# Kernel optimization log

Hardware: AMD Instinct MI355X
Metric: run time of the kernel (lower is better)

The kernel has to match this reference:

```python
import jax, jax.numpy as jnp
import numpy as np

N, D, K, P = 4096, 256, 16, 3
MAXDEG = K + 1          # self loop guarantees deg >= 1, randint caps deg <= K+1
TAU, LAM, BETA, MARGIN = 0.8, 0.5, 1.0, 0.1
EPS_PD = 1e-6           # F.pairwise_distance eps (added to the difference)


def _make_adj(k):
    nbr = jax.random.randint(k, (N, K), 0, N)
    m = jnp.zeros((N, N), jnp.float32)
    m = m.at[jnp.arange(N)[:, None], nbr].set(1.0)
    m = m.at[jnp.arange(N), jnp.arange(N)].set(1.0)
    return m / m.sum(1, keepdims=True)  # row-normalized metapath adjacency


def setup_inputs():
    key = jax.random.key(0)
    ks = jax.random.split(key, 12)
    g = 1.414 * (2.0 / (D + D)) ** 0.5  # xavier_normal gain=1.414
    return {
        "h": jax.random.normal(ks[0], (N, D), jnp.float32),
        "mps": jnp.stack([_make_adj(ks[1 + i]) for i in range(P)]),
        "W_gcn": jax.random.normal(ks[4], (P, D, D), jnp.float32) * g,
        "b_gcn": jnp.zeros((P, D), jnp.float32),
        "prelu_a": jnp.full((P,), 0.25, jnp.float32),
        "att_fc_W": jax.random.normal(ks[5], (D, D), jnp.float32) * g,
        "att_fc_b": jnp.zeros((D,), jnp.float32),
        "att_vec": jax.random.normal(ks[6], (D,), jnp.float32) * g,
        "proj_W1": jax.random.normal(ks[7], (D, D), jnp.float32) * g,
        "proj_b1": jnp.zeros((D,), jnp.float32),
        "proj_W2": jax.random.normal(ks[8], (D, D), jnp.float32) * g,
        "proj_b2": jnp.zeros((D,), jnp.float32),
    }


def _gcn(h, adj, W, b, a):
    out = adj @ (h @ W.T) + b          # spmm(adj, fc(h)) + bias
    return jnp.where(out > 0, out, a * out)  # PReLU


def _node_loss(emb, adj):
    # vectorized form of the per-node nonzero/pairwise_distance loop
    mask = adj > 0                      # [N, N]
    deg = mask.sum(1)                   # [N], >= 1 via self loops
    # stable argsort: neighbors first (ascending index), matching torch.nonzero order
    pos_idx = jnp.argsort(~mask, axis=1)[:, :MAXDEG]
    neg_idx = jnp.argsort(mask, axis=1)[:, :MAXDEG]   # first deg non-neighbors
    anc = emb[:, None, :]               # anchor expanded over pairs
    dp = jnp.sum((anc - emb[pos_idx] + EPS_PD) ** 2, -1)  # [N, MAXDEG]
    dn = jnp.sum((anc - emb[neg_idx] + EPS_PD) ** 2, -1)
    valid = jnp.arange(MAXDEG)[None, :] < deg[:, None]
    per = jnp.maximum(dp - dn + MARGIN, 0.0) * valid
    return jnp.sum(per.sum(1) / deg.astype(emb.dtype))  # per-node mean, summed


def _proj(z, W1, b1, W2, b2):
    return jax.nn.elu(z @ W1.T + b1) @ W2.T + b2


def _contrast(z1, z2, pos, W1, b1, W2, b2):
    p1 = _proj(z1, W1, b1, W2, b2)
    p2 = _proj(z2, W1, b1, W2, b2)
    n1 = jnp.linalg.norm(p1, axis=-1, keepdims=True)
    n2 = jnp.linalg.norm(p2, axis=-1, keepdims=True)
    sim = jnp.exp((p1 @ p2.T) / (n1 * n2.T) / TAU)     # [N, N]
    m12 = sim / (sim.sum(1, keepdims=True) + 1e-8)
    m21 = sim.T / (sim.T.sum(1, keepdims=True) + 1e-8)
    l12 = -jnp.log((m12 * pos).sum(-1)).mean()
    l21 = -jnp.log((m21 * pos).sum(-1)).mean()
    return LAM * l12 + (1.0 - LAM) * l21


def reference(h, mps, W_gcn, b_gcn, prelu_a, att_fc_W, att_fc_b, att_vec,
              proj_W1, proj_b1, proj_W2, proj_b2):
    embeds = [_gcn(h, mps[i], W_gcn[i], b_gcn[i], prelu_a[i]) for i in range(P)]
    node_loss = sum(_node_loss(embeds[i], mps[i]) for i in range(P))
    # faithful to original control flow: i==0 inner loop overwrites self.loss,
    # so only the (0, P-1) pair survives from i==0
    closs = _contrast(embeds[0], embeds[P - 1], mps[0], proj_W1, proj_b1, proj_W2, proj_b2)
    for i in range(1, P - 1):
        for j in range(i + 1, P):
            closs = closs + _contrast(embeds[i], embeds[j], mps[i], proj_W1, proj_b1, proj_W2, proj_b2)
    # semantic attention over metapaths
    sp = jnp.stack([jnp.tanh(e @ att_fc_W.T + att_fc_b).mean(0) for e in embeds])  # [P, D]
    beta = jax.nn.softmax(sp @ att_vec)                                            # [P]
    z_mp = jnp.einsum('p,pnd->nd', beta, jnp.stack(embeds))
    return z_mp, node_loss + BETA * closs
```

## Files before the change

### kernel.cpp

```cpp
#include <hip/hip_runtime.h>
#include <hip/hip_bf16.h>

constexpr int N = 4096;
constexpr int D = 256;
constexpr int P = 3;
constexpr int MAXDEG = 17;
constexpr float TAU = 0.8f;
constexpr float MARGIN = 0.1f;
constexpr float EPS_PD = 1e-6f;

constexpr int LDP = 40;
constexpr int LDK = 72;

constexpr int OFF_H    = 0;
constexpr int OFF_WG   = 1048576;
constexpr int OFF_ATTW = 1245184;
constexpr int OFF_W1   = 1310720;
constexpr int OFF_W2   = 1376256;
constexpr int OFF_BG   = 1441792;
constexpr int OFF_ATTB = 1442560;
constexpr int OFF_AV   = 1442816;
constexpr int OFF_PA   = 1443072;
constexpr int OFF_B1   = 1443328;
constexpr int OFF_B2   = 1443584;
constexpr int CONV_TOTAL = 1443840;

typedef __attribute__((ext_vector_type(8))) short bfrag8;
typedef __attribute__((ext_vector_type(4))) float facc4;

__device__ inline facc4 mfma16(bfrag8 a, bfrag8 b, facc4 c) {
    return __builtin_amdgcn_mfma_f32_16x16x32_bf16(a, b, c, 0, 0, 0);
}
__device__ inline float b2f(__hip_bfloat16 v) { return __bfloat162float(v); }
__device__ inline float bfbits2f(unsigned short u) {
    return __uint_as_float(((unsigned int)u) << 16);
}
__device__ inline unsigned short f2bfbits(float v) {
    __hip_bfloat16 t = __float2bfloat16(v);
    return *(unsigned short*)&t;
}
__device__ inline int get_bf(const int* __restrict__ counter) { return counter[0] > 100; }

__device__ inline float load_in(const void* p, size_t i, int bf) {
    return bf ? __bfloat162float(((const __hip_bfloat16*)p)[i])
              : ((const float*)p)[i];
}

__global__ void detect_dtype(const unsigned int* __restrict__ w, int nwords,
                             int* __restrict__ counter) {
    int stride = gridDim.x * blockDim.x;
    int c = 0;
    for (int i = blockIdx.x * blockDim.x + threadIdx.x; i < nwords; i += stride) {
        unsigned int x = w[i];
        if ((x & 0xFFFF0000u) == 0u && x != 0u) c++;
    }
    for (int s = 32; s > 0; s >>= 1) c += __shfl_down(c, s);
    if ((threadIdx.x & 63) == 0 && c > 0) atomicAdd(counter, c);
}

__global__ void convert_all(const void* h, const void* wg, const void* attw,
                            const void* w1, const void* w2, const void* bg,
                            const void* attb, const void* av, const void* pa,
                            const void* b1, const void* b2,
                            const int* __restrict__ counter,
                            __hip_bfloat16* __restrict__ dst) {
    int bf = get_bf(counter);
    const void* srcs[11] = {h, wg, attw, w1, w2, bg, attb, av, pa, b1, b2};
    const int offs[11] = {OFF_H, OFF_WG, OFF_ATTW, OFF_W1, OFF_W2, OFF_BG,
                          OFF_ATTB, OFF_AV, OFF_PA, OFF_B1, OFF_B2};
    const int lens[11] = {1048576, 196608, 65536, 65536, 65536, 768, 256, 256, 3, 256, 256};
    int stride = gridDim.x * blockDim.x;
    int t0 = blockIdx.x * blockDim.x + threadIdx.x;
    #pragma unroll
    for (int s = 0; s < 11; s++) {
        for (int i = t0; i < lens[s]; i += stride)
            dst[offs[s] + i] = __float2bfloat16(load_in(srcs[s], i, bf));
    }
}

__global__ void extract_sparse(const void* __restrict__ mps, const int* __restrict__ counter,
                               int* __restrict__ nbr_idx, float* __restrict__ nbr_val,
                               int* __restrict__ neg_idx, int* __restrict__ deg) {
    int bf = get_bf(counter);
    int row = blockIdx.x;
    int t = threadIdx.x;
    __shared__ int cnt;
    __shared__ int sidx[32];
    __shared__ float sval[32];
    if (t == 0) cnt = 0;
    __syncthreads();
    int e0 = t * 16;
    if (bf) {
        const uint4* base = (const uint4*)((const __hip_bfloat16*)mps + (size_t)row * N + e0);
        #pragma unroll
        for (int v = 0; v < 2; v++) {
            uint4 w = base[v];
            unsigned int ws[4] = {w.x, w.y, w.z, w.w};
            #pragma unroll
            for (int j = 0; j < 4; j++) {
                unsigned short lo = (unsigned short)(ws[j] & 0xFFFFu);
                unsigned short hi = (unsigned short)(ws[j] >> 16);
                if (lo) { int k = atomicAdd(&cnt, 1); if (k < 32) { sidx[k] = e0 + v * 8 + j * 2;     sval[k] = bfbits2f(lo); } }
                if (hi) { int k = atomicAdd(&cnt, 1); if (k < 32) { sidx[k] = e0 + v * 8 + j * 2 + 1; sval[k] = bfbits2f(hi); } }
            }
        }
    } else {
        const float4* base = (const float4*)((const float*)mps + (size_t)row * N + e0);
        #pragma unroll
        for (int v = 0; v < 4; v++) {
            float4 w = base[v];
            float ws[4] = {w.x, w.y, w.z, w.w};
            #pragma unroll
            for (int j = 0; j < 4; j++)
                if (ws[j] > 0.f) { int k = atomicAdd(&cnt, 1); if (k < 32) { sidx[k] = e0 + v * 4 + j; sval[k] = ws[j]; } }
        }
    }
    __syncthreads();
    if (t == 0) {
        int dg = cnt; if (dg > MAXDEG) dg = MAXDEG;
        for (int i = 1; i < dg; i++) {
            int ki = sidx[i]; float kv = sval[i]; int j = i - 1;
            while (j >= 0 && sidx[j] > ki) { sidx[j+1] = sidx[j]; sval[j+1] = sval[j]; j--; }
            sidx[j+1] = ki; sval[j+1] = kv;
        }
        deg[row] = dg;
        int* oi = nbr_idx + (size_t)row * MAXDEG;
        float* ov = nbr_val + (size_t)row * MAXDEG;
        int* ng = neg_idx + (size_t)row * MAXDEG;
        for (int i = 0; i < MAXDEG; i++) { oi[i] = (i < dg) ? sidx[i] : 0; ov[i] = (i < dg) ? sval[i] : 0.f; }
        int c = 0, j = 0, found = 0;
        while (found < MAXDEG) {
            if (j < dg && sidx[j] == c) { j++; c++; continue; }
            ng[found++] = c++;
        }
    }
}

template <int ACT>
__global__ void gemm_mfma(const __hip_bfloat16* __restrict__ Abase, size_t strideA,
                          const __hip_bfloat16* __restrict__ Bbase, size_t strideB,
                          const __hip_bfloat16* __restrict__ bias, size_t strideBias,
                          __hip_bfloat16* __restrict__ Cbase, size_t strideC) {
    int z = blockIdx.z;
    const __hip_bfloat16* A = Abase + (size_t)z * strideA;
    const __hip_bfloat16* B = Bbase + (size_t)z * strideB;
    __shared__ __align__(16) __hip_bfloat16 As[64 * LDP];
    __shared__ __align__(16) __hip_bfloat16 Bs[64 * LDP];
    int bm = blockIdx.x * 64, bn = blockIdx.y * 64;
    int tid = threadIdx.x, wave = tid >> 6, lane = tid & 63;
    int quad = lane >> 4, l15 = lane & 15;
    int wr = (wave & 1) * 32, wc = (wave >> 1) * 32;
    facc4 acc[2][2] = {};
    int sr = tid >> 2, kq = (tid & 3) * 8;
    for (int k0 = 0; k0 < D; k0 += 32) {
        *(bfrag8*)&As[sr * LDP + kq] = *(const bfrag8*)&A[(size_t)(bm + sr) * D + k0 + kq];
        *(bfrag8*)&Bs[sr * LDP + kq] = *(const bfrag8*)&B[(size_t)(bn + sr) * D + k0 + kq];
        __syncthreads();
        bfrag8 af[2], bfr[2];
        #pragma unroll
        for (int mi = 0; mi < 2; mi++)
            af[mi] = *(const bfrag8*)&As[(wr + mi * 16 + l15) * LDP + quad * 8];
        #pragma unroll
        for (int ni = 0; ni < 2; ni++)
            bfr[ni] = *(const bfrag8*)&Bs[(wc + ni * 16 + l15) * LDP + quad * 8];
        #pragma unroll
        for (int mi = 0; mi < 2; mi++)
            #pragma unroll
            for (int ni = 0; ni < 2; ni++)
                acc[mi][ni] = mfma16(af[mi], bfr[ni], acc[mi][ni]);
        __syncthreads();
    }
    #pragma unroll
    for (int mi = 0; mi < 2; mi++) {
        #pragma unroll
        for (int ni = 0; ni < 2; ni++) {
            int col = bn + wc + ni * 16 + l15;
            #pragma unroll
            for (int r = 0; r < 4; r++) {
                int row = bm + wr + mi * 16 + quad * 4 + r;
                float v = acc[mi][ni][r];
                if (bias) v += b2f(bias[col]);
                if (ACT == 1) v = v > 0.f ? v : expm1f(v);
                Cbase[(size_t)z * strideC + (size_t)row * D + col] = __float2bfloat16(v);
            }
        }
    }
}

__global__ void gemm_dual(const __hip_bfloat16* __restrict__ embBase,
                          const __hip_bfloat16* __restrict__ conv,
                          __hip_bfloat16* __restrict__ xbuf,
                          float* __restrict__ spacc) {
    int z = blockIdx.z;
    const __hip_bfloat16* A = embBase + (size_t)z * N * D;
    const __hip_bfloat16* Ba = conv + OFF_ATTW;
    const __hip_bfloat16* Bw = conv + OFF_W1;
    __shared__ __align__(16) __hip_bfloat16 As[64 * LDP];
    __shared__ __align__(16) __hip_bfloat16 Bsa[64 * LDP];
    __shared__ __align__(16) __hip_bfloat16 Bsw[64 * LDP];
    int bm = blockIdx.x * 64, bn = blockIdx.y * 64;
    int tid = threadIdx.x, wave = tid >> 6, lane = tid & 63;
    int quad = lane >> 4, l15 = lane & 15;
    int wr = (wave & 1) * 32, wc = (wave >> 1) * 32;
    facc4 accA[2][2] = {};
    facc4 accW[2][2] = {};
    int sr = tid >> 2, kq = (tid & 3) * 8;
    for (int k0 = 0; k0 < D; k0 += 32) {
        *(bfrag8*)&As[sr * LDP + kq]  = *(const bfrag8*)&A[(size_t)(bm + sr) * D + k0 + kq];
        *(bfrag8*)&Bsa[sr * LDP + kq] = *(const bfrag8*)&Ba[(size_t)(bn + sr) * D + k0 + kq];
        *(bfrag8*)&Bsw[sr * LDP + kq] = *(const bfrag8*)&Bw[(size_t)(bn + sr) * D + k0 + kq];
        __syncthreads();
        bfrag8 af[2], ba[2], bw[2];
        #pragma unroll
        for (int mi = 0; mi < 2; mi++)
            af[mi] = *(const bfrag8*)&As[(wr + mi * 16 + l15) * LDP + quad * 8];
        #pragma unroll
        for (int ni = 0; ni < 2; ni++) {
            ba[ni] = *(const bfrag8*)&Bsa[(wc + ni * 16 + l15) * LDP + quad * 8];
            bw[ni] = *(const bfrag8*)&Bsw[(wc + ni * 16 + l15) * LDP + quad * 8];
        }
        #pragma unroll
        for (int mi = 0; mi < 2; mi++)
            #pragma unroll
            for (int ni = 0; ni < 2; ni++) {
                accA[mi][ni] = mfma16(af[mi], ba[ni], accA[mi][ni]);
                accW[mi][ni] = mfma16(af[mi], bw[ni], accW[mi][ni]);
            }
        __syncthreads();
    }
    float cs[2] = {0.f, 0.f};
    #pragma unroll
    for (int mi = 0; mi < 2; mi++) {
        #pragma unroll
        for (int ni = 0; ni < 2; ni++) {
            int col = bn + wc + ni * 16 + l15;
            float battb = b2f(conv[OFF_ATTB + col]);
            float bb1   = b2f(conv[OFF_B1 + col]);
            #pragma unroll
            for (int r = 0; r < 4; r++) {
                int row = bm + wr + mi * 16 + quad * 4 + r;
                cs[ni] += tanhf(accA[mi][ni][r] + battb);
                float v = accW[mi][ni][r] + bb1;
                v = v > 0.f ? v : expm1f(v);
                xbuf[(size_t)z * N * D + (size_t)row * D + col] = __float2bfloat16(v);
            }
        }
    }
    #pragma unroll
    for (int ni = 0; ni < 2; ni++) {
        float v = cs[ni];
        v += __shfl_xor(v, 16); v += __shfl_xor(v, 32);
        if (quad == 0) {
            int col = bn + wc + ni * 16 + l15;
            atomicAdd(&spacc[(size_t)z * D + col], v);
        }
    }
}

__global__ void gemm_w2_norm(const __hip_bfloat16* __restrict__ xbase,
                             const __hip_bfloat16* __restrict__ conv,
                             __hip_bfloat16* __restrict__ qbase) {
    int z = blockIdx.z;
    const __hip_bfloat16* A = xbase + (size_t)z * N * D;
    const __hip_bfloat16* B = conv + OFF_W2;
    __shared__ __align__(16) __hip_bfloat16 As[16 * LDP];
    __shared__ __align__(16) __hip_bfloat16 Bs[256 * LDP];
    __shared__ float sred[4][16];
    int bm = blockIdx.x * 16;
    int tid = threadIdx.x, wave = tid >> 6, lane = tid & 63;
    int quad = lane >> 4, l15 = lane & 15;
    int wc = wave * 64;
    facc4 acc[4] = {};
    for (int k0 = 0; k0 < D; k0 += 32) {
        if (tid < 64) {
            int r = tid >> 2, kq = (tid & 3) * 8;
            *(bfrag8*)&As[r * LDP + kq] = *(const bfrag8*)&A[(size_t)(bm + r) * D + k0 + kq];
        }
        #pragma unroll
        for (int i = 0; i < 4; i++) {
            int f = tid + 256 * i;
            int r = f >> 2, kq = (f & 3) * 8;
            *(bfrag8*)&Bs[r * LDP + kq] = *(const bfrag8*)&B[(size_t)r * D + k0 + kq];
        }
        __syncthreads();
        bfrag8 af = *(const bfrag8*)&As[l15 * LDP + quad * 8];
        #pragma unroll
        for (int ni = 0; ni < 4; ni++) {
            bfrag8 bf = *(const bfrag8*)&Bs[(wc + ni * 16 + l15) * LDP + quad * 8];
            acc[ni] = mfma16(af, bf, acc[ni]);
        }
        __syncthreads();
    }
    float vv[4][4];
    #pragma unroll
    for (int ni = 0; ni < 4; ni++) {
        float bb = b2f(conv[OFF_B2 + wc + ni * 16 + l15]);
        #pragma unroll
        for (int r = 0; r < 4; r++) vv[ni][r] = acc[ni][r] + bb;
    }
    #pragma unroll
    for (int r = 0; r < 4; r++) {
        float ss = vv[0][r] * vv[0][r] + vv[1][r] * vv[1][r] +
                   vv[2][r] * vv[2][r] + vv[3][r] * vv[3][r];
        ss += __shfl_xor(ss, 1); ss += __shfl_xor(ss, 2);
        ss += __shfl_xor(ss, 4); ss += __shfl_xor(ss, 8);
        if (l15 == 0) sred[wave][quad * 4 + r] = ss;
    }
    __syncthreads();
    #pragma unroll
    for (int r = 0; r < 4; r++) {
        int rl = quad * 4 + r;
        float ssum = sred[0][rl] + sred[1][rl] + sred[2][rl] + sred[3][rl];
        float inv = rsqrtf(ssum + 1e-30f);
        int row = bm + rl;
        #pragma unroll
        for (int ni = 0; ni < 4; ni++)
            qbase[(size_t)z * N * D + (size_t)row * D + wc + ni * 16 + l15] =
                __float2bfloat16(vv[ni][r] * inv);
    }
}

__global__ void spmm_prelu(const __hip_bfloat16* __restrict__ Xbase,
                           const int* __restrict__ nbr_idx, const float* __restrict__ nbr_val,
                           const int* __restrict__ deg, const __hip_bfloat16* __restrict__ conv,
                           __hip_bfloat16* __restrict__ embBase) {
    int z = blockIdx.z;
    int wave = threadIdx.x >> 6, lane = threadIdx.x & 63;
    int n = blockIdx.x * 4 + wave;
    const __hip_bfloat16* X = Xbase + (size_t)z * N * D;
    const int* idx = nbr_idx + ((size_t)z * N + n) * MAXDEG;
    const float* val = nbr_val + ((size_t)z * N + n) * MAXDEG;
    int dg = deg[z * N + n];
    float acc[4] = {0.f, 0.f, 0.f, 0.f};
    for (int k = 0; k < dg; k++) {
        int j = idx[k];
        float vk = val[k];
        ushort4 x = *(const ushort4*)&X[(size_t)j * D + lane * 4];
        acc[0] += vk * bfbits2f(x.x); acc[1] += vk * bfbits2f(x.y);
        acc[2] += vk * bfbits2f(x.z); acc[3] += vk * bfbits2f(x.w);
    }
    ushort4 bb = *(const ushort4*)&conv[OFF_BG + z * D + lane * 4];
    float b[4] = {bfbits2f(bb.x), bfbits2f(bb.y), bfbits2f(bb.z), bfbits2f(bb.w)};
    float a = b2f(conv[OFF_PA + z]);
    ushort4 o;
    float v0 = acc[0] + b[0]; o.x = f2bfbits(v0 > 0.f ? v0 : a * v0);
    float v1 = acc[1] + b[1]; o.y = f2bfbits(v1 > 0.f ? v1 : a * v1);
    float v2 = acc[2] + b[2]; o.z = f2bfbits(v2 > 0.f ? v2 : a * v2);
    float v3 = acc[3] + b[3]; o.w = f2bfbits(v3 > 0.f ? v3 : a * v3);
    *(ushort4*)&embBase[(size_t)z * N * D + (size_t)n * D + lane * 4] = o;
}

__global__ void sim_mfma(const __hip_bfloat16* __restrict__ q,
                         float* __restrict__ rowsum, float* __restrict__ colsum) {
    int pair = blockIdx.z;
    const __hip_bfloat16* Qa = q + (size_t)pair * N * D;
    const __hip_bfloat16* Qb = q + (size_t)2 * N * D;
    __shared__ __align__(16) __hip_bfloat16 As[128 * LDK];
    __shared__ __align__(16) __hip_bfloat16 Bs[128 * LDK];
    int bm = blockIdx.x * 128, bn = blockIdx.y * 128;
    int tid = threadIdx.x, wave = tid >> 6, lane = tid & 63;
    int quad = lane >> 4, l15 = lane & 15;
    int wr = (wave & 1) * 64, wc = (wave >> 1) * 64;
    facc4 acc[4][4] = {};
    int sr0 = tid >> 3, kq = (tid & 7) * 8;
    for (int k0 = 0; k0 < D; k0 += 64) {
        #pragma unroll
        for (int i = 0; i < 4; i++) {
            int r = sr0 + 32 * i;
            *(bfrag8*)&As[r * LDK + kq] = *(const bfrag8*)&Qa[(size_t)(bm + r) * D + k0 + kq];
            *(bfrag8*)&Bs[r * LDK + kq] = *(const bfrag8*)&Qb[(size_t)(bn + r) * D + k0 + kq];
        }
        __syncthreads();
        #pragma unroll
        for (int kk = 0; kk < 64; kk += 32) {
            bfrag8 af[4], bfr[4];
            #pragma unroll
            for (int mi = 0; mi < 4; mi++)
                af[mi] = *(const bfrag8*)&As[(wr + mi * 16 + l15) * LDK + kk + quad * 8];
            #pragma unroll
            for (int ni = 0; ni < 4; ni++)
                bfr[ni] = *(const bfrag8*)&Bs[(wc + ni * 16 + l15) * LDK + kk + quad * 8];
            #pragma unroll
            for (int mi = 0; mi < 4; mi++)
                #pragma unroll
                for (int ni = 0; ni < 4; ni++)
                    acc[mi][ni] = mfma16(af[mi], bfr[ni], acc[mi][ni]);
        }
        __syncthreads();
    }
    constexpr float invtau = 1.0f / TAU;
    float rs[4][4];
    float cs[4] = {0.f, 0.f, 0.f, 0.f};
    #pragma unroll
    for (int mi = 0; mi < 4; mi++)
        #pragma unroll
        for (int r = 0; r < 4; r++) rs[mi][r] = 0.f;
    #pragma unroll
    for (int mi = 0; mi < 4; mi++)
        #pragma unroll
        for (int ni = 0; ni < 4; ni++)
            #pragma unroll
            for (int r = 0; r < 4; r++) {
                float e = __expf(acc[mi][ni][r] * invtau);
                rs[mi][r] += e;
                cs[ni] += e;
            }
    #pragma unroll
    for (int mi = 0; mi < 4; mi++)
        #pragma unroll
        for (int r = 0; r < 4; r++) {
            float v = rs[mi][r];
            v += __shfl_xor(v, 1); v += __shfl_xor(v, 2);
            v += __shfl_xor(v, 4); v += __shfl_xor(v, 8);
            rs[mi][r] = v;
        }
    if (l15 == 0) {
        #pragma unroll
        for (int mi = 0; mi < 4; mi++)
            #pragma unroll
            for (int r = 0; r < 4; r++)
                atomicAdd(&rowsum[(size_t)pair * N + bm + wr + mi * 16 + quad * 4 + r], rs[mi][r]);
    }
    #pragma unroll
    for (int ni = 0; ni < 4; ni++) {
        float v = cs[ni];
        v += __shfl_xor(v, 16); v += __shfl_xor(v, 32);
        if (quad == 0)
            atomicAdd(&colsum[(size_t)pair * N + bn + wc + ni * 16 + l15], v);
    }
}

__global__ void posdot(const __hip_bfloat16* __restrict__ q,
                       const int* __restrict__ nbr_idx, const float* __restrict__ nbr_val,
                       const int* __restrict__ deg,
                       float* __restrict__ pdrow, float* __restrict__ pdcol) {
    int pair = blockIdx.z;
    int wave = threadIdx.x >> 6, lane = threadIdx.x & 63;
    int n = blockIdx.x * 4 + wave;
    const __hip_bfloat16* Qa = q + (size_t)pair * N * D;
    const __hip_bfloat16* Qb = q + (size_t)2 * N * D;
    int dg = deg[pair * N + n];
    const int* idx = nbr_idx + ((size_t)pair * N + n) * MAXDEG;
    const float* val = nbr_val + ((size_t)pair * N + n) * MAXDEG;
    const float invtau = 1.0f / TAU;
    ushort4 ar = *(const ushort4*)&Qa[(size_t)n * D + lane * 4];
    ushort4 br = *(const ushort4*)&Qb[(size_t)n * D + lane * 4];
    float a[4] = {bfbits2f(ar.x), bfbits2f(ar.y), bfbits2f(ar.z), bfbits2f(ar.w)};
    float b[4] = {bfbits2f(br.x), bfbits2f(br.y), bfbits2f(br.z), bfbits2f(br.w)};
    float sr = 0.f, sc = 0.f;
    for (int k = 0; k < dg; k++) {
        int j = idx[k];
        ushort4 pj = *(const ushort4*)&Qb[(size_t)j * D + lane * 4];
        ushort4 aj = *(const ushort4*)&Qa[(size_t)j * D + lane * 4];
        float dr = a[0] * bfbits2f(pj.x) + a[1] * bfbits2f(pj.y) +
                   a[2] * bfbits2f(pj.z) + a[3] * bfbits2f(pj.w);
        float dc = b[0] * bfbits2f(aj.x) + b[1] * bfbits2f(aj.y) +
                   b[2] * bfbits2f(aj.z) + b[3] * bfbits2f(aj.w);
        #pragma unroll
        for (int s = 1; s <= 32; s <<= 1) { dr += __shfl_xor(dr, s); dc += __shfl_xor(dc, s); }
        sr += __expf(dr * invtau) * val[k];
        sc += __expf(dc * invtau) * val[k];
    }
    if (lane == 0) { pdrow[pair * N + n] = sr; pdcol[pair * N + n] = sc; }
}

__global__ void node_loss_k(const __hip_bfloat16* __restrict__ embBase,
                            const int* __restrict__ nbr_idx, const int* __restrict__ neg_idx,
                            const int* __restrict__ deg, float* __restrict__ nlpart) {
    int z = blockIdx.z;
    int wave = threadIdx.x >> 6, lane = threadIdx.x & 63;
    int n = blockIdx.x * 4 + wave;
    const __hip_bfloat16* emb = embBase + (size_t)z * N * D;
    int dg = deg[z * N + n];
    const int* ip = nbr_idx + ((size_t)z * N + n) * MAXDEG;
    const int* ig = neg_idx + ((size_t)z * N + n) * MAXDEG;
    ushort4 ar = *(const ushort4*)&emb[(size_t)n * D + lane * 4];
    float a[4] = {bfbits2f(ar.x), bfbits2f(ar.y), bfbits2f(ar.z), bfbits2f(ar.w)};
    float s = 0.f;
    for (int k = 0; k < dg; k++) {
        int jp = ip[k], jn = ig[k];
        ushort4 pr = *(const ushort4*)&emb[(size_t)jp * D + lane * 4];
        ushort4 nr = *(const ushort4*)&emb[(size_t)jn * D + lane * 4];
        float pv[4] = {bfbits2f(pr.x), bfbits2f(pr.y), bfbits2f(pr.z), bfbits2f(pr.w)};
        float nv[4] = {bfbits2f(nr.x), bfbits2f(nr.y), bfbits2f(nr.z), bfbits2f(nr.w)};
        float dp = 0.f, dn = 0.f;
        #pragma unroll
        for (int i = 0; i < 4; i++) {
            float x = a[i] - pv[i] + EPS_PD; dp += x * x;
            float y = a[i] - nv[i] + EPS_PD; dn += y * y;
        }
        #pragma unroll
        for (int st = 1; st <= 32; st <<= 1) { dp += __shfl_xor(dp, st); dn += __shfl_xor(dn, st); }
        float v = dp - dn + MARGIN;
        s += v > 0.f ? v : 0.f;
    }
    if (lane == 0) nlpart[z * N + n] = s / (float)dg;
}

__global__ void reduce_loss_beta(const float* __restrict__ nlpart,
                                 const float* __restrict__ rowsum, const float* __restrict__ colsum,
                                 const float* __restrict__ pdrow, const float* __restrict__ pdcol,
                                 const float* __restrict__ spacc,
                                 const __hip_bfloat16* __restrict__ conv,
                                 float* __restrict__ beta, float* __restrict__ loss) {
    int t = threadIdx.x;
    __shared__ float red[256];
    __shared__ float w[P];
    for (int p = 0; p < P; p++) {
        float v = (spacc[p * D + t] / (float)N) * b2f(conv[OFF_AV + t]);
        red[t] = v;
        __syncthreads();
        for (int s = 128; s > 0; s >>= 1) { if (t < s) red[t] += red[t + s]; __syncthreads(); }
        if (t == 0) w[p] = red[0];
        __syncthreads();
    }
    float s = 0.f;
    for (int i = t; i < P * N; i += 256) s += nlpart[i];
    for (int i = t; i < 2 * N; i += 256) {
        float l12 = -logf(pdrow[i] / (rowsum[i] + 1e-8f));
        float l21 = -logf(pdcol[i] / (colsum[i] + 1e-8f));
        s += (0.5f * l12 + 0.5f * l21) / (float)N;
    }
    red[t] = s;
    __syncthreads();
    for (int st = 128; st > 0; st >>= 1) { if (t < st) red[t] += red[t + st]; __syncthreads(); }
    if (t == 0) {
        loss[0] = red[0];
        float m = fmaxf(w[0], fmaxf(w[1], w[2]));
        float e0 = __expf(w[0] - m), e1 = __expf(w[1] - m), e2 = __expf(w[2] - m);
        float ssum = e0 + e1 + e2;
        beta[0] = e0 / ssum; beta[1] = e1 / ssum; beta[2] = e2 / ssum;
    }
}

__global__ void zmp_out(const __hip_bfloat16* __restrict__ embBase, const float* __restrict__ beta,
                        const float* __restrict__ loss, const int* __restrict__ counter,
                        void* __restrict__ out) {
    int bf = get_bf(counter);
    int i = blockIdx.x * 256 + threadIdx.x;
    float v = beta[0] * b2f(embBase[i]) + beta[1] * b2f(embBase[(size_t)N * D + i]) +
              beta[2] * b2f(embBase[(size_t)2 * N * D + i]);
    if (bf) {
        __hip_bfloat16* o = (__hip_bfloat16*)out;
        o[i] = __float2bfloat16(v);
        if (i == 0) o[(size_t)N * D] = __float2bfloat16(*loss);
    } else {
        float* o = (float*)out;
        o[i] = v;
        if (i == 0) o[(size_t)N * D] = *loss;
    }
}

extern "C" void kernel_launch(void* const* d_in, const int* in_sizes, int n_in,
                              void* d_out, int out_size, void* d_ws, size_t ws_size,
                              hipStream_t stream) {
    const void* h        = d_in[0];
    const void* mps      = d_in[1];
    const void* W_gcn    = d_in[2];
    const void* b_gcn    = d_in[3];
    const void* prelu_a  = d_in[4];
    const void* att_fc_W = d_in[5];
    const void* att_fc_b = d_in[6];
    const void* att_vec  = d_in[7];
    const void* proj_W1  = d_in[8];
    const void* proj_b1  = d_in[9];
    const void* proj_W2  = d_in[10];
    const void* proj_b2  = d_in[11];

    char* ws = (char*)d_ws;
    size_t off = 0;
    auto alloc = [&](size_t bytes) -> char* {
        char* p = ws + off;
        off = (off + bytes + 255) & ~(size_t)255;
        return p;
    };
    __hip_bfloat16* conv = (__hip_bfloat16*)alloc((size_t)CONV_TOTAL * 2);
    __hip_bfloat16* xbuf = (__hip_bfloat16*)alloc((size_t)P * N * D * 2);
    __hip_bfloat16* emb  = (__hip_bfloat16*)alloc((size_t)P * N * D * 2);
    __hip_bfloat16* q    = (__hip_bfloat16*)alloc((size_t)P * N * D * 2);
    int*   nbr_idx = (int*)alloc((size_t)P * N * MAXDEG * 4);
    float* nbr_val = (float*)alloc((size_t)P * N * MAXDEG * 4);
    int*   neg_idx = (int*)alloc((size_t)P * N * MAXDEG * 4);
    int*   deg     = (int*)alloc((size_t)P * N * 4);
    float* nlpart  = (float*)alloc((size_t)P * N * 4);
    float* pdrow   = (float*)alloc((size_t)2 * N * 4);
    float* pdcol   = (float*)alloc((size_t)2 * N * 4);
    char* zero_begin = ws + off;
    float* rowsum = (float*)alloc((size_t)2 * N * 4);
    float* colsum = (float*)alloc((size_t)2 * N * 4);
    float* spacc  = (float*)alloc((size_t)P * D * 4);
    float* beta   = (float*)alloc(16);
    float* loss   = (float*)alloc(16);
    int*   counter = (int*)alloc(16);
    size_t zero_bytes = (size_t)((ws + off) - zero_begin);
    hipMemsetAsync(zero_begin, 0, zero_bytes, stream);

    detect_dtype<<<1024, 256, 0, stream>>>((const unsigned int*)mps, 2 * 1024 * 1024, counter);

    convert_all<<<512, 256, 0, stream>>>(h, W_gcn, att_fc_W, proj_W1, proj_W2, b_gcn,
                                         att_fc_b, att_vec, prelu_a, proj_b1, proj_b2,
                                         counter, conv);

    extract_sparse<<<P * N, 256, 0, stream>>>(mps, counter, nbr_idx, nbr_val, neg_idx, deg);

    dim3 ggrid(N / 64, D / 64, P);
    size_t nd = (size_t)N * D;
    gemm_mfma<0><<<ggrid, 256, 0, stream>>>(
        conv + OFF_H, 0, conv + OFF_WG, (size_t)D * D, nullptr, 0, xbuf, nd);
    spmm_prelu<<<dim3(N / 4, 1, P), 256, 0, stream>>>(xbuf, nbr_idx, nbr_val, deg, conv, emb);
    gemm_dual<<<ggrid, 256, 0, stream>>>(emb, conv, xbuf, spacc);
    gemm_w2_norm<<<dim3(N / 16, 1, P), 256, 0, stream>>>(xbuf, conv, q);
    sim_mfma<<<dim3(N / 128, N / 128, 2), 256, 0, stream>>>(q, rowsum, colsum);
    posdot<<<dim3(N / 4, 1, 2), 256, 0, stream>>>(q, nbr_idx, nbr_val, deg, pdrow, pdcol);
    node_loss_k<<<dim3(N / 4, 1, P), 256, 0, stream>>>(emb, nbr_idx, neg_idx, deg, nlpart);
    reduce_loss_beta<<<1, 256, 0, stream>>>(nlpart, rowsum, colsum, pdrow, pdcol,
                                            spacc, conv, beta, loss);
    zmp_out<<<(N * D) / 256, 256, 0, stream>>>(emb, beta, loss, counter, d_out);
}
```

Before: 507.8 us.

## Use direct global-to-LDS loads with XOR swizzle in sim GEMM; merge edge kernels

The similarity GEMM now stages Q tiles with global_load_lds 16-byte transfers straight into LDS, using an XOR-swizzled unpadded layout instead of padded rows. This removes the register round-trip and uses the swizzle to avoid LDS bank conflicts. Separately, the posdot and node_loss kernels are merged into one launch over P+2 z-slices, which saves a kernel launch and lets the two gather workloads share the GPU. The swizzle indexing must match between store and read, and 16-byte global_load_lds support is hardware-specific.

```diff
diff --git a/kernel.cpp b/kernel.cpp
--- a/kernel.cpp
+++ b/kernel.cpp
@@ -10,7 +10,6 @@
 constexpr float EPS_PD = 1e-6f;
 
 constexpr int LDP = 40;
-constexpr int LDK = 72;
 
 constexpr int OFF_H    = 0;
 constexpr int OFF_WG   = 1048576;
@@ -44,6 +43,12 @@
 __device__ inline float load_in(const void* p, size_t i, int bf) {
     return bf ? __bfloat162float(((const __hip_bfloat16*)p)[i])
               : ((const float*)p)[i];
+}
+
+__device__ __forceinline__ void gl_lds16(const __hip_bfloat16* g, __hip_bfloat16* l) {
+    __builtin_amdgcn_global_load_lds(
+        (const __attribute__((address_space(1))) unsigned int*)g,
+        (__attribute__((address_space(3))) unsigned int*)l, 16, 0, 0);
 }
 
 __global__ void detect_dtype(const unsigned int* __restrict__ w, int nwords,
@@ -355,31 +360,40 @@
     int pair = blockIdx.z;
     const __hip_bfloat16* Qa = q + (size_t)pair * N * D;
     const __hip_bfloat16* Qb = q + (size_t)2 * N * D;
-    __shared__ __align__(16) __hip_bfloat16 As[128 * LDK];
-    __shared__ __align__(16) __hip_bfloat16 Bs[128 * LDK];
+    __shared__ __align__(16) __hip_bfloat16 As[128 * 64];
+    __shared__ __align__(16) __hip_bfloat16 Bs[128 * 64];
     int bm = blockIdx.x * 128, bn = blockIdx.y * 128;
     int tid = threadIdx.x, wave = tid >> 6, lane = tid & 63;
     int quad = lane >> 4, l15 = lane & 15;
     int wr = (wave & 1) * 64, wc = (wave >> 1) * 64;
     facc4 acc[4][4] = {};
-    int sr0 = tid >> 3, kq = (tid & 7) * 8;
+    int sr0 = tid >> 3;
+    int cc  = tid & 7;
     for (int k0 = 0; k0 < D; k0 += 64) {
         #pragma unroll
         for (int i = 0; i < 4; i++) {
             int r = sr0 + 32 * i;
-            *(bfrag8*)&As[r * LDK + kq] = *(const bfrag8*)&Qa[(size_t)(bm + r) * D + k0 + kq];
-            *(bfrag8*)&Bs[r * LDK + kq] = *(const bfrag8*)&Qb[(size_t)(bn + r) * D + k0 + kq];
+            int cg = (cc ^ (r & 7)) * 8;
+            gl_lds16(&Qa[(size_t)(bm + r) * D + k0 + cg], &As[r * 64 + cc * 8]);
+            gl_lds16(&Qb[(size_t)(bn + r) * D + k0 + cg], &Bs[r * 64 + cc * 8]);
         }
         __syncthreads();
         #pragma unroll
         for (int kk = 0; kk < 64; kk += 32) {
+            int kb = kk >> 3;
             bfrag8 af[4], bfr[4];
             #pragma unroll
-            for (int mi = 0; mi < 4; mi++)
-                af[mi] = *(const bfrag8*)&As[(wr + mi * 16 + l15) * LDK + kk + quad * 8];
-            #pragma unroll
-            for (int ni = 0; ni < 4; ni++)
-                bfr[ni] = *(const bfrag8*)&Bs[(wc + ni * 16 + l15) * LDK + kk + quad * 8];
+            for (int mi = 0; mi < 4; mi++) {
+                int R = wr + mi * 16 + l15;
+                int pc = ((kb + quad) ^ (l15 & 7)) * 8;
+                af[mi] = *(const bfrag8*)&As[R * 64 + pc];
+            }
+            #pragma unroll
+            for (int ni = 0; ni < 4; ni++) {
+                int R = wc + ni * 16 + l15;
+                int pc = ((kb + quad) ^ (l15 & 7)) * 8;
+                bfr[ni] = *(const bfrag8*)&Bs[R * 64 + pc];
+            }
             #pragma unroll
             for (int mi = 0; mi < 4; mi++)
                 #pragma unroll
@@ -430,71 +444,68 @@
     }
 }
 
-__global__ void posdot(const __hip_bfloat16* __restrict__ q,
-                       const int* __restrict__ nbr_idx, const float* __restrict__ nbr_val,
-                       const int* __restrict__ deg,
-                       float* __restrict__ pdrow, float* __restrict__ pdcol) {
-    int pair = blockIdx.z;
-    int wave = threadIdx.x >> 6, lane = threadIdx.x & 63;
-    int n = blockIdx.x * 4 + wave;
-    const __hip_bfloat16* Qa = q + (size_t)pair * N * D;
-    const __hip_bfloat16* Qb = q + (size_t)2 * N * D;
-    int dg = deg[pair * N + n];
-    const int* idx = nbr_idx + ((size_t)pair * N + n) * MAXDEG;
-    const float* val = nbr_val + ((size_t)pair * N + n) * MAXDEG;
-    const float invtau = 1.0f / TAU;
-    ushort4 ar = *(const ushort4*)&Qa[(size_t)n * D + lane * 4];
-    ushort4 br = *(const ushort4*)&Qb[(size_t)n * D + lane * 4];
-    float a[4] = {bfbits2f(ar.x), bfbits2f(ar.y), bfbits2f(ar.z), bfbits2f(ar.w)};
-    float b[4] = {bfbits2f(br.x), bfbits2f(br.y), bfbits2f(br.z), bfbits2f(br.w)};
-    float sr = 0.f, sc = 0.f;
-    for (int k = 0; k < dg; k++) {
-        int j = idx[k];
-        ushort4 pj = *(const ushort4*)&Qb[(size_t)j * D + lane * 4];
-        ushort4 aj = *(const ushort4*)&Qa[(size_t)j * D + lane * 4];
-        float dr = a[0] * bfbits2f(pj.x) + a[1] * bfbits2f(pj.y) +
-                   a[2] * bfbits2f(pj.z) + a[3] * bfbits2f(pj.w);
-        float dc = b[0] * bfbits2f(aj.x) + b[1] * bfbits2f(aj.y) +
-                   b[2] * bfbits2f(aj.z) + b[3] * bfbits2f(aj.w);
-        #pragma unroll
-        for (int s = 1; s <= 32; s <<= 1) { dr += __shfl_xor(dr, s); dc += __shfl_xor(dc, s); }
-        sr += __expf(dr * invtau) * val[k];
-        sc += __expf(dc * invtau) * val[k];
-    }
-    if (lane == 0) { pdrow[pair * N + n] = sr; pdcol[pair * N + n] = sc; }
-}
-
-__global__ void node_loss_k(const __hip_bfloat16* __restrict__ embBase,
-                            const int* __restrict__ nbr_idx, const int* __restrict__ neg_idx,
-                            const int* __restrict__ deg, float* __restrict__ nlpart) {
+__global__ void edge_losses(const __hip_bfloat16* __restrict__ embBase,
+                            const __hip_bfloat16* __restrict__ q,
+                            const int* __restrict__ nbr_idx, const float* __restrict__ nbr_val,
+                            const int* __restrict__ neg_idx, const int* __restrict__ deg,
+                            float* __restrict__ nlpart,
+                            float* __restrict__ pdrow, float* __restrict__ pdcol) {
     int z = blockIdx.z;
     int wave = threadIdx.x >> 6, lane = threadIdx.x & 63;
     int n = blockIdx.x * 4 + wave;
-    const __hip_bfloat16* emb = embBase + (size_t)z * N * D;
-    int dg = deg[z * N + n];
-    const int* ip = nbr_idx + ((size_t)z * N + n) * MAXDEG;
-    const int* ig = neg_idx + ((size_t)z * N + n) * MAXDEG;
-    ushort4 ar = *(const ushort4*)&emb[(size_t)n * D + lane * 4];
-    float a[4] = {bfbits2f(ar.x), bfbits2f(ar.y), bfbits2f(ar.z), bfbits2f(ar.w)};
-    float s = 0.f;
-    for (int k = 0; k < dg; k++) {
-        int jp = ip[k], jn = ig[k];
-        ushort4 pr = *(const ushort4*)&emb[(size_t)jp * D + lane * 4];
-        ushort4 nr = *(const ushort4*)&emb[(size_t)jn * D + lane * 4];
-        float pv[4] = {bfbits2f(pr.x), bfbits2f(pr.y), bfbits2f(pr.z), bfbits2f(pr.w)};
-        float nv[4] = {bfbits2f(nr.x), bfbits2f(nr.y), bfbits2f(nr.z), bfbits2f(nr.w)};
-        float dp = 0.f, dn = 0.f;
-        #pragma unroll
-        for (int i = 0; i < 4; i++) {
-            float x = a[i] - pv[i] + EPS_PD; dp += x * x;
-            float y = a[i] - nv[i] + EPS_PD; dn += y * y;
-        }
-        #pragma unroll
-        for (int st = 1; st <= 32; st <<= 1) { dp += __shfl_xor(dp, st); dn += __shfl_xor(dn, st); }
-        float v = dp - dn + MARGIN;
-        s += v > 0.f ? v : 0.f;
-    }
-    if (lane == 0) nlpart[z * N + n] = s / (float)dg;
+    if (z < P) {
+        const __hip_bfloat16* emb = embBase + (size_t)z * N * D;
+        int dg = deg[z * N + n];
+        const int* ip = nbr_idx + ((size_t)z * N + n) * MAXDEG;
+        const int* ig = neg_idx + ((size_t)z * N + n) * MAXDEG;
+        ushort4 ar = *(const ushort4*)&emb[(size_t)n * D + lane * 4];
+        float a[4] = {bfbits2f(ar.x), bfbits2f(ar.y), bfbits2f(ar.z), bfbits2f(ar.w)};
+        float s = 0.f;
+        for (int k = 0; k < dg; k++) {
+            int jp = ip[k], jn = ig[k];
+            ushort4 pr = *(const ushort4*)&emb[(size_t)jp * D + lane * 4];
+            ushort4 nr = *(const ushort4*)&emb[(size_t)jn * D + lane * 4];
+            float dp = 0.f, dn = 0.f;
+            float x0 = a[0] - bfbits2f(pr.x) + EPS_PD, y0 = a[0] - bfbits2f(nr.x) + EPS_PD;
+            float x1 = a[1] - bfbits2f(pr.y) + EPS_PD, y1 = a[1] - bfbits2f(nr.y) + EPS_PD;
+            float x2 = a[2] - bfbits2f(pr.z) + EPS_PD, y2 = a[2] - bfbits2f(nr.z) + EPS_PD;
+            float x3 = a[3] - bfbits2f(pr.w) + EPS_PD, y3 = a[3] - bfbits2f(nr.w) + EPS_PD;
+            dp = x0 * x0 + x1 * x1 + x2 * x2 + x3 * x3;
+            dn = y0 * y0 + y1 * y1 + y2 * y2 + y3 * y3;
+            #pragma unroll
+            for (int st = 1; st <= 32; st <<= 1) { dp += __shfl_xor(dp, st); dn += __shfl_xor(dn, st); }
+            float v = dp - dn + MARGIN;
+            s += v > 0.f ? v : 0.f;
+        }
+        if (lane == 0) nlpart[z * N + n] = s / (float)dg;
+    } else {
+        int pair = z - P;
+        const __hip_bfloat16* Qa = q + (size_t)pair * N * D;
+        const __hip_bfloat16* Qb = q + (size_t)2 * N * D;
+        int dg = deg[pair * N + n];
+        const int* idx = nbr_idx + ((size_t)pair * N + n) * MAXDEG;
+        const float* val = nbr_val + ((size_t)pair * N + n) * MAXDEG;
+        const float invtau = 1.0f / TAU;
+        ushort4 ar = *(const ushort4*)&Qa[(size_t)n * D + lane * 4];
+        ushort4 br = *(const ushort4*)&Qb[(size_t)n * D + lane * 4];
+        float a[4] = {bfbits2f(ar.x), bfbits2f(ar.y), bfbits2f(ar.z), bfbits2f(ar.w)};
+        float b[4] = {bfbits2f(br.x), bfbits2f(br.y), bfbits2f(br.z), bfbits2f(br.w)};
+        float sr = 0.f, sc = 0.f;
+        for (int k = 0; k < dg; k++) {
+            int j = idx[k];
+            ushort4 pj = *(const ushort4*)&Qb[(size_t)j * D + lane * 4];
+            ushort4 aj = *(const ushort4*)&Qa[(size_t)j * D + lane * 4];
+            float dr = a[0] * bfbits2f(pj.x) + a[1] * bfbits2f(pj.y) +
+                       a[2] * bfbits2f(pj.z) + a[3] * bfbits2f(pj.w);
+            float dc = b[0] * bfbits2f(aj.x) + b[1] * bfbits2f(aj.y) +
+                       b[2] * bfbits2f(aj.z) + b[3] * bfbits2f(aj.w);
+            #pragma unroll
+            for (int s = 1; s <= 32; s <<= 1) { dr += __shfl_xor(dr, s); dc += __shfl_xor(dc, s); }
+            sr += __expf(dr * invtau) * val[k];
+            sc += __expf(dc * invtau) * val[k];
+        }
+        if (lane == 0) { pdrow[pair * N + n] = sr; pdcol[pair * N + n] = sc; }
+    }
 }
 
 __global__ void reduce_loss_beta(const float* __restrict__ nlpart,
@@ -611,8 +622,8 @@
     gemm_dual<<<ggrid, 256, 0, stream>>>(emb, conv, xbuf, spacc);
     gemm_w2_norm<<<dim3(N / 16, 1, P), 256, 0, stream>>>(xbuf, conv, q);
     sim_mfma<<<dim3(N / 128, N / 128, 2), 256, 0, stream>>>(q, rowsum, colsum);
-    posdot<<<dim3(N / 4, 1, 2), 256, 0, stream>>>(q, nbr_idx, nbr_val, deg, pdrow, pdcol);
-    node_loss_k<<<dim3(N / 4, 1, P), 256, 0, stream>>>(emb, nbr_idx, neg_idx, deg, nlpart);
+    edge_losses<<<dim3(N / 4, 1, P + 2), 256, 0, stream>>>(emb, q, nbr_idx, nbr_val,
+                                                           neg_idx, deg, nlpart, pdrow, pdcol);
     reduce_loss_beta<<<1, 256, 0, stream>>>(nlpart, rowsum, colsum, pdrow, pdcol,
                                             spacc, conv, beta, loss);
     zmp_out<<<(N * D) / 256, 256, 0, stream>>>(emb, beta, loss, counter, d_out);
```

New measurement: 499.3 us. About the same (-1.7%).
